# Performance work log

Measured on AMD Instinct MI355X. Metric: run time of the kernel, lower is better.

Reference implementation:

```python
import jax, jax.numpy as jnp
import numpy as np
from jax import lax

R = 2  # upscale factor


def setup_inputs() -> dict:
    key = jax.random.key(0)
    k1, k2, k3 = jax.random.split(key, 3)
    x = jax.random.normal(k1, (16, 192, 192, 64), dtype=jnp.float32)
    # Conv2D kernel: HWIO, filters = r*r*64 = 256
    W = jax.random.normal(k2, (3, 3, 64, 256), dtype=jnp.float32) * 0.05
    b = jax.random.normal(k3, (256,), dtype=jnp.float32) * 0.05
    return {"x": x, "W": W, "b": b}


def reference(x, W, b):
    # Conv2D, stride 1, 'same' padding, NHWC/HWIO
    y = lax.conv_general_dilated(
        x, W, window_strides=(1, 1), padding="SAME",
        dimension_numbers=("NHWC", "HWIO", "NHWC")) + b
    # phase_shift: O[B, i*r+q, j*r+p, k] = y[B, i, j, k*r*r + p*r + q]
    B, a, bdim, c = y.shape
    cp = c // (R * R)
    y = y.reshape(B, a, bdim, cp, R, R)          # [B,a,b,k,p,q]
    y = jnp.transpose(y, (0, 1, 5, 2, 4, 3))     # [B,a,q,b,p,k]
    return y.reshape(B, a * R, bdim * R, cp)
```

## Files before the change

### kernel.cpp

```cpp
#include <hip/hip_runtime.h>
#include <stdint.h>

typedef short bf16x8 __attribute__((ext_vector_type(8)));
typedef float f32x4  __attribute__((ext_vector_type(4)));

#define GLOAD_LDS16(gp, lp) \
    __builtin_amdgcn_global_load_lds((const __attribute__((address_space(1))) void*)(gp), \
                                     (__attribute__((address_space(3))) void*)(lp), 16, 0, 0)

__device__ __forceinline__ uint32_t bfbits(float f) {
    uint32_t u = __builtin_bit_cast(uint32_t, f);
    u += 0x7FFFu + ((u >> 16) & 1u);
    return u >> 16;
}
__device__ __forceinline__ uint32_t pk2(float a, float b) {
    return bfbits(a) | (bfbits(b) << 16);
}

__global__ void prep_kernel(const float* __restrict__ x, short* __restrict__ xb,
                            const float* __restrict__ W, short* __restrict__ Wt) {
    const int b = blockIdx.x;
    if (b < 2048) {
        const int total = 16 * 194 * 194 * 8;
        for (int i = b * 256 + threadIdx.x; i < total; i += 2048 * 256) {
            int g  = i & 7;
            int t  = i >> 3;
            int wp = t % 194; t /= 194;
            int hp = t % 194;
            int nn = t / 194;
            uint4 r = {0u, 0u, 0u, 0u};
            if (hp >= 1 && hp <= 192 && wp >= 1 && wp <= 192) {
                const float* s = x + (((size_t)nn * 192 + (hp - 1)) * 192 + (wp - 1)) * 64 + g * 8;
                f32x4 a = __builtin_nontemporal_load((const f32x4*)s);
                f32x4 bb = __builtin_nontemporal_load((const f32x4*)(s + 4));
                r.x = pk2(a[0], a[1]); r.y = pk2(a[2], a[3]);
                r.z = pk2(bb[0], bb[1]); r.w = pk2(bb[2], bb[3]);
            }
            *(uint4*)(xb + (size_t)i * 8) = r;
        }
    } else {
        int idx = (b - 2048) * 256 + threadIdx.x;
        if (idx < 147456) {
            int t  = idx >> 14;
            int r  = idx & 16383;
            int c  = r >> 12;
            int j  = (r >> 6) & 63;
            int ic = r & 63;
            Wt[idx] = (short)bfbits(W[(t * 64 + ic) * 256 + j * 4 + c]);
        }
    }
}

#define NRING 7
#define ASLOT_B 8448
#define B_OFF   (NRING * ASLOT_B)
#define SMEM_SHORTS ((B_OFF + 2 * 8192) / 2)

__global__ __launch_bounds__(256, 2) void conv_ps_kernel(
    const short* __restrict__ xb, const short* __restrict__ Wt,
    const float* __restrict__ bias, float* __restrict__ out)
{
    __shared__ short smem[SMEM_SHORTS];

    const int tid   = threadIdx.x;
    const int lane  = tid & 63;
    const int wv    = tid >> 6;
    const int row_l = lane & 15;
    const int grp   = lane >> 4;
    const int b7    = row_l & 7;

    const int raw = blockIdx.x;
    const int lb  = (raw & 7) * 192 + (raw >> 3);
    const int c    = lb & 3;
    const int wt   = (lb >> 2) % 3;
    const int hseg = (lb / 12) % 8;
    const int n    = lb / 96;
    const int w0   = wt * 64;
    const int hbase = hseg * 24;
    const int q = c & 1, p = (c >> 1) & 1;

    const short* wsrc = Wt + c * 4096;

    auto issueB = [&](int tap, int buf) {
        #pragma unroll
        for (int r = 0; r < 2; ++r) {
            int cch = tid + r * 256;
            int j = cch >> 3, s = cch & 7, ss = s ^ (j & 7);
            GLOAD_LDS16(wsrc + tap * 16384 + j * 64 + ss * 8,
                        (char*)smem + B_OFF + buf * 8192 + (wv * 64 + r * 256) * 16);
        }
    };
    auto issueA = [&](int row) {
        int rowc = row > 192 ? 192 : row;
        int slot = (row + 1) % NRING;
        size_t rbase = ((size_t)n * 194 + (rowc + 1)) * 194;
        #pragma unroll
        for (int r = 0; r < 2; ++r) {
            int cch = wv * 132 + r * 64 + lane;
            int wpos = cch >> 3, g = cch & 7, gs = g ^ (wpos & 7);
            GLOAD_LDS16(xb + (rbase + (w0 + wpos)) * 64 + gs * 8,
                        (char*)smem + slot * ASLOT_B + (wv * 132 + r * 64) * 16);
        }
        if (lane < 4) {
            int cch = wv * 132 + 128 + lane;
            int wpos = cch >> 3, g = cch & 7, gs = g ^ (wpos & 7);
            GLOAD_LDS16(xb + (rbase + (w0 + wpos)) * 64 + gs * 8,
                        (char*)smem + slot * ASLOT_B + (wv * 132 + 128) * 16);
        }
    };

    issueB(0, 0);
    #pragma unroll
    for (int r = 0; r < 5; ++r) issueA(hbase - 1 + r);
    asm volatile("s_waitcnt vmcnt(0)" ::: "memory");
    __builtin_amdgcn_sched_barrier(0);
    __syncthreads();

    f32x4 bv4[4];
    #pragma unroll
    for (int nt = 0; nt < 4; ++nt) {
        const int j0 = nt * 16 + grp * 4;
        #pragma unroll
        for (int jv = 0; jv < 4; ++jv)
            bv4[nt][jv] = bias[(j0 + jv) * 4 + c];
    }

    f32x4 accA[4][4], accB[4][4];

#define SCHB __builtin_amdgcn_sched_barrier(0)

#define COMPUTE_TAP(ACC, DY, DX, BUF) { \
    const int rd = row_l + (DX); \
    const int a7 = rd & 7; \
    const int aB = sl[DY] * 4224 + rd * 64; \
    const short* bbase = smem + B_OFF / 2 + (BUF) * 4096 + row_l * 64; \
    _Pragma("unroll") for (int ks = 0; ks < 2; ++ks) { \
        const int kg = ks * 4 + grp; \
        const short* ap = &smem[aB + ((kg ^ a7) << 3)]; \
        const short* bp = bbase + ((kg ^ b7) << 3); \
        bf16x8 af[4], bfr[4]; \
        _Pragma("unroll") for (int mt = 0; mt < 4; ++mt) af[mt]  = *(const bf16x8*)(ap + mt * 1024); \
        _Pragma("unroll") for (int nt = 0; nt < 4; ++nt) bfr[nt] = *(const bf16x8*)(bp + nt * 1024); \
        _Pragma("unroll") for (int mt = 0; mt < 4; ++mt) \
            _Pragma("unroll") for (int nt = 0; nt < 4; ++nt) \
                ACC[mt][nt] = __builtin_amdgcn_mfma_f32_16x16x32_bf16( \
                    bfr[nt], af[mt], ACC[mt][nt], 0, 0, 0); \
    } }

#define ST2(ACCO, S) { \
    const int mt_ = (S) >> 1, n0_ = ((S) & 1) * 2; \
    float* po_ = out + ((rowb_o + 2 * (w0 + mt_ * 16 + row_l) + p) * 64 + grp * 4); \
    __builtin_nontemporal_store(ACCO[mt_][n0_],     (f32x4*)(po_ + n0_ * 16)); \
    __builtin_nontemporal_store(ACCO[mt_][n0_ + 1], (f32x4*)(po_ + (n0_ + 1) * 16)); }

#define TAPX(ACC, K, DY, DX, PAR, VM, EXTRA, STS) \
    __builtin_amdgcn_s_barrier(); SCHB; \
    issueB(((K) + 1) % 9, ((PAR) + (K) + 1) & 1); \
    EXTRA; SCHB; \
    STS; SCHB; \
    asm volatile("s_waitcnt vmcnt(" #VM ")" ::: "memory"); SCHB; \
    __builtin_amdgcn_s_barrier(); SCHB; \
    COMPUTE_TAP(ACC, DY, DX, ((PAR) + (K)) & 1)

#define TILE_HEAD(ACC, ITV) \
    const int h0 = hbase + (ITV) * 4; \
    int sl[3]; \
    _Pragma("unroll") for (int dy = 0; dy < 3; ++dy) sl[dy] = (h0 + wv + dy) % NRING; \
    _Pragma("unroll") for (int i = 0; i < 4; ++i) \
        _Pragma("unroll") for (int j = 0; j < 4; ++j) ACC[i][j] = bv4[j];

#define STEADY_TILE(ACC, ACCO, ITV, PAR) { \
    TILE_HEAD(ACC, ITV); \
    const long rowb_o = ((long)(n * 384 + 2 * (h0 - 4 + wv) + q)) * 384; \
    TAPX(ACC, 0, 0, 0, PAR, 10, { issueA(h0 + 4); issueA(h0 + 5); }, ST2(ACCO, 0)); \
    TAPX(ACC, 1, 0, 1, PAR, 12, {}, ST2(ACCO, 1)); \
    TAPX(ACC, 2, 0, 2, PAR,  6, {}, ST2(ACCO, 2)); \
    TAPX(ACC, 3, 1, 0, PAR,  9, { issueA(h0 + 6); }, ST2(ACCO, 3)); \
    TAPX(ACC, 4, 1, 1, PAR,  9, {}, ST2(ACCO, 4)); \
    TAPX(ACC, 5, 1, 2, PAR,  6, {}, ST2(ACCO, 5)); \
    TAPX(ACC, 6, 2, 0, PAR,  9, { issueA(h0 + 7); }, ST2(ACCO, 6)); \
    TAPX(ACC, 7, 2, 1, PAR,  9, {}, ST2(ACCO, 7)); \
    TAPX(ACC, 8, 2, 2, PAR,  4, {}, {}); }

    {
        TILE_HEAD(accA, 0);
        TAPX(accA, 0, 0, 0, 0, 8, { issueA(h0 + 4); issueA(h0 + 5); }, {});
        TAPX(accA, 1, 0, 1, 0, 8, {}, {});
        TAPX(accA, 2, 0, 2, 0, 2, {}, {});
        TAPX(accA, 3, 1, 0, 0, 5, { issueA(h0 + 6); }, {});
        TAPX(accA, 4, 1, 1, 0, 5, {}, {});
        TAPX(accA, 5, 1, 2, 0, 2, {}, {});
        TAPX(accA, 6, 2, 0, 0, 5, { issueA(h0 + 7); }, {});
        TAPX(accA, 7, 2, 1, 0, 5, {}, {});
        TAPX(accA, 8, 2, 2, 0, 2, {}, {});
    }
    #pragma unroll 1
    for (int it2 = 1; it2 < 5; it2 += 2) {
        STEADY_TILE(accB, accA, it2, 1);
        STEADY_TILE(accA, accB, it2 + 1, 0);
    }
    STEADY_TILE(accB, accA, 5, 1);
    {
        const int h = hbase + 20 + wv;
        const long rowb = ((long)(n * 384 + 2 * h + q)) * 384;
        #pragma unroll
        for (int mt = 0; mt < 4; ++mt) {
            float* po = out + ((rowb + 2 * (w0 + mt * 16 + row_l) + p) * 64 + grp * 4);
            #pragma unroll
            for (int nt = 0; nt < 4; ++nt)
                __builtin_nontemporal_store(accB[mt][nt], (f32x4*)(po + nt * 16));
        }
    }
#undef STEADY_TILE
#undef TILE_HEAD
#undef TAPX
#undef ST2
#undef COMPUTE_TAP
#undef SCHB
}

extern "C" void kernel_launch(void* const* d_in, const int* in_sizes, int n_in,
                              void* d_out, int out_size, void* d_ws, size_t ws_size,
                              hipStream_t stream) {
    const float* x = (const float*)d_in[0];
    const float* W = (const float*)d_in[1];
    const float* b = (const float*)d_in[2];
    float* out = (float*)d_out;

    const size_t xb_bytes = (size_t)16 * 194 * 194 * 64 * 2;
    short* xbuf = (short*)d_ws;
    short* Wt   = (short*)((char*)d_ws + xb_bytes);

    hipLaunchKernelGGL(prep_kernel, dim3(2624), dim3(256), 0, stream, x, xbuf, W, Wt);
    hipLaunchKernelGGL(conv_ps_kernel, dim3(1536), dim3(256), 0, stream, xbuf, Wt, b, out);
}
```

Measured before the change: 223.4 us.

## Prefetch next tap's A fragments from LDS into double-buffered registers

Splits the per-tap LDS reads so that the A (input) fragments for the next filter tap are read into a second register set while the current tap's MFMAs run. The two sets alternate between taps, and the first tap of each tile is prefetched at the end of the previous tile. The aim is to hide LDS read latency behind MFMA execution within the barrier-separated tap schedule. In exchange, live VGPRs rise by about 64 registers. That risks lower occupancy or spills, and the early reads must not run ahead of the vmcnt waits that guard the ring buffer.

```diff
diff --git a/kernel.cpp b/kernel.cpp
--- a/kernel.cpp
+++ b/kernel.cpp
@@ -126,25 +126,18 @@
     }
 
     f32x4 accA[4][4], accB[4][4];
+    bf16x8 af0[2][4], af1[2][4];
 
 #define SCHB __builtin_amdgcn_sched_barrier(0)
 
-#define COMPUTE_TAP(ACC, DY, DX, BUF) { \
-    const int rd = row_l + (DX); \
-    const int a7 = rd & 7; \
-    const int aB = sl[DY] * 4224 + rd * 64; \
-    const short* bbase = smem + B_OFF / 2 + (BUF) * 4096 + row_l * 64; \
+#define READ_AF(DST, SLOT, DX) { \
+    const int rd_ = row_l + (DX); \
+    const int a7_ = rd_ & 7; \
+    const int aB_ = (SLOT) * 4224 + rd_ * 64; \
     _Pragma("unroll") for (int ks = 0; ks < 2; ++ks) { \
-        const int kg = ks * 4 + grp; \
-        const short* ap = &smem[aB + ((kg ^ a7) << 3)]; \
-        const short* bp = bbase + ((kg ^ b7) << 3); \
-        bf16x8 af[4], bfr[4]; \
-        _Pragma("unroll") for (int mt = 0; mt < 4; ++mt) af[mt]  = *(const bf16x8*)(ap + mt * 1024); \
-        _Pragma("unroll") for (int nt = 0; nt < 4; ++nt) bfr[nt] = *(const bf16x8*)(bp + nt * 1024); \
-        _Pragma("unroll") for (int mt = 0; mt < 4; ++mt) \
-            _Pragma("unroll") for (int nt = 0; nt < 4; ++nt) \
-                ACC[mt][nt] = __builtin_amdgcn_mfma_f32_16x16x32_bf16( \
-                    bfr[nt], af[mt], ACC[mt][nt], 0, 0, 0); \
+        const short* ap_ = &smem[aB_ + (((ks * 4 + grp) ^ a7_) << 3)]; \
+        _Pragma("unroll") for (int mt_ = 0; mt_ < 4; ++mt_) \
+            DST[ks][mt_] = *(const bf16x8*)(ap_ + mt_ * 1024); \
     } }
 
 #define ST2(ACCO, S) { \
@@ -153,53 +146,74 @@
     __builtin_nontemporal_store(ACCO[mt_][n0_],     (f32x4*)(po_ + n0_ * 16)); \
     __builtin_nontemporal_store(ACCO[mt_][n0_ + 1], (f32x4*)(po_ + (n0_ + 1) * 16)); }
 
-#define TAPX(ACC, K, DY, DX, PAR, VM, EXTRA, STS) \
+#define TAPX(ACC, K, PAR, VM, EXTRA, STS, AFC, AFN, NSLOT, NDX) \
     __builtin_amdgcn_s_barrier(); SCHB; \
     issueB(((K) + 1) % 9, ((PAR) + (K) + 1) & 1); \
     EXTRA; SCHB; \
     STS; SCHB; \
     asm volatile("s_waitcnt vmcnt(" #VM ")" ::: "memory"); SCHB; \
     __builtin_amdgcn_s_barrier(); SCHB; \
-    COMPUTE_TAP(ACC, DY, DX, ((PAR) + (K)) & 1)
+    { \
+        bf16x8 bfr[2][4]; \
+        const short* bbase_ = smem + B_OFF / 2 + ((((PAR) + (K)) & 1)) * 4096 + row_l * 64; \
+        _Pragma("unroll") for (int ks = 0; ks < 2; ++ks) { \
+            const short* bp_ = bbase_ + (((ks * 4 + grp) ^ b7) << 3); \
+            _Pragma("unroll") for (int nt_ = 0; nt_ < 4; ++nt_) \
+                bfr[ks][nt_] = *(const bf16x8*)(bp_ + nt_ * 1024); \
+        } \
+        READ_AF(AFN, NSLOT, NDX); \
+        _Pragma("unroll") for (int ks = 0; ks < 2; ++ks) \
+            _Pragma("unroll") for (int mt_ = 0; mt_ < 4; ++mt_) \
+                _Pragma("unroll") for (int nt_ = 0; nt_ < 4; ++nt_) \
+                    ACC[mt_][nt_] = __builtin_amdgcn_mfma_f32_16x16x32_bf16( \
+                        bfr[ks][nt_], AFC[ks][mt_], ACC[mt_][nt_], 0, 0, 0); \
+    }
 
 #define TILE_HEAD(ACC, ITV) \
     const int h0 = hbase + (ITV) * 4; \
     int sl[3]; \
     _Pragma("unroll") for (int dy = 0; dy < 3; ++dy) sl[dy] = (h0 + wv + dy) % NRING; \
+    const int nsl0 = (h0 + 4 + wv) % NRING; \
+    (void)nsl0; \
     _Pragma("unroll") for (int i = 0; i < 4; ++i) \
         _Pragma("unroll") for (int j = 0; j < 4; ++j) ACC[i][j] = bv4[j];
 
-#define STEADY_TILE(ACC, ACCO, ITV, PAR) { \
+#define STEADY_TILE(ACC, ACCO, ITV, PAR, AFE, AFO) { \
     TILE_HEAD(ACC, ITV); \
     const long rowb_o = ((long)(n * 384 + 2 * (h0 - 4 + wv) + q)) * 384; \
-    TAPX(ACC, 0, 0, 0, PAR, 10, { issueA(h0 + 4); issueA(h0 + 5); }, ST2(ACCO, 0)); \
-    TAPX(ACC, 1, 0, 1, PAR, 12, {}, ST2(ACCO, 1)); \
-    TAPX(ACC, 2, 0, 2, PAR,  6, {}, ST2(ACCO, 2)); \
-    TAPX(ACC, 3, 1, 0, PAR,  9, { issueA(h0 + 6); }, ST2(ACCO, 3)); \
-    TAPX(ACC, 4, 1, 1, PAR,  9, {}, ST2(ACCO, 4)); \
-    TAPX(ACC, 5, 1, 2, PAR,  6, {}, ST2(ACCO, 5)); \
-    TAPX(ACC, 6, 2, 0, PAR,  9, { issueA(h0 + 7); }, ST2(ACCO, 6)); \
-    TAPX(ACC, 7, 2, 1, PAR,  9, {}, ST2(ACCO, 7)); \
-    TAPX(ACC, 8, 2, 2, PAR,  4, {}, {}); }
+    TAPX(ACC, 0, PAR, 10, { issueA(h0 + 4); issueA(h0 + 5); }, ST2(ACCO, 0), AFE, AFO, sl[0], 1); \
+    TAPX(ACC, 1, PAR, 12, {}, ST2(ACCO, 1), AFO, AFE, sl[0], 2); \
+    TAPX(ACC, 2, PAR,  6, {}, ST2(ACCO, 2), AFE, AFO, sl[1], 0); \
+    TAPX(ACC, 3, PAR,  9, { issueA(h0 + 6); }, ST2(ACCO, 3), AFO, AFE, sl[1], 1); \
+    TAPX(ACC, 4, PAR,  9, {}, ST2(ACCO, 4), AFE, AFO, sl[1], 2); \
+    TAPX(ACC, 5, PAR,  6, {}, ST2(ACCO, 5), AFO, AFE, sl[2], 0); \
+    TAPX(ACC, 6, PAR,  9, { issueA(h0 + 7); }, ST2(ACCO, 6), AFE, AFO, sl[2], 1); \
+    TAPX(ACC, 7, PAR,  9, {}, ST2(ACCO, 7), AFO, AFE, sl[2], 2); \
+    TAPX(ACC, 8, PAR,  4, {}, {}, AFE, AFO, nsl0, 0); }
+
+    {
+        const int psl = (hbase + wv) % NRING;
+        READ_AF(af0, psl, 0);
+    }
 
     {
         TILE_HEAD(accA, 0);
-        TAPX(accA, 0, 0, 0, 0, 8, { issueA(h0 + 4); issueA(h0 + 5); }, {});
-        TAPX(accA, 1, 0, 1, 0, 8, {}, {});
-        TAPX(accA, 2, 0, 2, 0, 2, {}, {});
-        TAPX(accA, 3, 1, 0, 0, 5, { issueA(h0 + 6); }, {});
-        TAPX(accA, 4, 1, 1, 0, 5, {}, {});
-        TAPX(accA, 5, 1, 2, 0, 2, {}, {});
-        TAPX(accA, 6, 2, 0, 0, 5, { issueA(h0 + 7); }, {});
-        TAPX(accA, 7, 2, 1, 0, 5, {}, {});
-        TAPX(accA, 8, 2, 2, 0, 2, {}, {});
+        TAPX(accA, 0, 0, 8, { issueA(h0 + 4); issueA(h0 + 5); }, {}, af0, af1, sl[0], 1);
+        TAPX(accA, 1, 0, 8, {}, {}, af1, af0, sl[0], 2);
+        TAPX(accA, 2, 0, 2, {}, {}, af0, af1, sl[1], 0);
+        TAPX(accA, 3, 0, 5, { issueA(h0 + 6); }, {}, af1, af0, sl[1], 1);
+        TAPX(accA, 4, 0, 5, {}, {}, af0, af1, sl[1], 2);
+        TAPX(accA, 5, 0, 2, {}, {}, af1, af0, sl[2], 0);
+        TAPX(accA, 6, 0, 5, { issueA(h0 + 7); }, {}, af0, af1, sl[2], 1);
+        TAPX(accA, 7, 0, 5, {}, {}, af1, af0, sl[2], 2);
+        TAPX(accA, 8, 0, 2, {}, {}, af0, af1, nsl0, 0);
     }
     #pragma unroll 1
     for (int it2 = 1; it2 < 5; it2 += 2) {
-        STEADY_TILE(accB, accA, it2, 1);
-        STEADY_TILE(accA, accB, it2 + 1, 0);
-    }
-    STEADY_TILE(accB, accA, 5, 1);
+        STEADY_TILE(accB, accA, it2, 1, af1, af0);
+        STEADY_TILE(accA, accB, it2 + 1, 0, af0, af1);
+    }
+    STEADY_TILE(accB, accA, 5, 1, af1, af0);
     {
         const int h = hbase + 20 + wv;
         const long rowb = ((long)(n * 384 + 2 * h + q)) * 384;
@@ -215,7 +229,7 @@
 #undef TILE_HEAD
 #undef TAPX
 #undef ST2
-#undef COMPUTE_TAP
+#undef READ_AF
 #undef SCHB
 }
 
```

Result: slower. 234.1 us (+4.8%).

## Fuse fp32-to-bf16 input conversion and padding into conv kernel via register staging

Applied to the files above, without the earlier changes.

Removes the separate prep pass that wrote a padded bf16 copy of the input. The conv kernel now loads fp32 rows into registers, converts and zero-pads them in-kernel, and writes them swizzled into the LDS ring, interleaved with MFMA taps under retuned waitcnt values. This saves a full read plus write of the activation tensor. In exchange it reads fp32 (twice the bytes per tile, with halo rows re-read by neighbouring blocks), uses 9 extra vector registers for staging, and adds VALU conversion work inside the main loop.

```diff
diff --git a/kernel.cpp b/kernel.cpp
--- a/kernel.cpp
+++ b/kernel.cpp
@@ -17,37 +17,15 @@
     return bfbits(a) | (bfbits(b) << 16);
 }
 
-__global__ void prep_kernel(const float* __restrict__ x, short* __restrict__ xb,
-                            const float* __restrict__ W, short* __restrict__ Wt) {
-    const int b = blockIdx.x;
-    if (b < 2048) {
-        const int total = 16 * 194 * 194 * 8;
-        for (int i = b * 256 + threadIdx.x; i < total; i += 2048 * 256) {
-            int g  = i & 7;
-            int t  = i >> 3;
-            int wp = t % 194; t /= 194;
-            int hp = t % 194;
-            int nn = t / 194;
-            uint4 r = {0u, 0u, 0u, 0u};
-            if (hp >= 1 && hp <= 192 && wp >= 1 && wp <= 192) {
-                const float* s = x + (((size_t)nn * 192 + (hp - 1)) * 192 + (wp - 1)) * 64 + g * 8;
-                f32x4 a = __builtin_nontemporal_load((const f32x4*)s);
-                f32x4 bb = __builtin_nontemporal_load((const f32x4*)(s + 4));
-                r.x = pk2(a[0], a[1]); r.y = pk2(a[2], a[3]);
-                r.z = pk2(bb[0], bb[1]); r.w = pk2(bb[2], bb[3]);
-            }
-            *(uint4*)(xb + (size_t)i * 8) = r;
-        }
-    } else {
-        int idx = (b - 2048) * 256 + threadIdx.x;
-        if (idx < 147456) {
-            int t  = idx >> 14;
-            int r  = idx & 16383;
-            int c  = r >> 12;
-            int j  = (r >> 6) & 63;
-            int ic = r & 63;
-            Wt[idx] = (short)bfbits(W[(t * 64 + ic) * 256 + j * 4 + c]);
-        }
+__global__ void wt_kernel(const float* __restrict__ W, short* __restrict__ Wt) {
+    int idx = blockIdx.x * 256 + threadIdx.x;
+    if (idx < 147456) {
+        int t  = idx >> 14;
+        int r  = idx & 16383;
+        int c  = r >> 12;
+        int j  = (r >> 6) & 63;
+        int ic = r & 63;
+        Wt[idx] = (short)bfbits(W[(t * 64 + ic) * 256 + j * 4 + c]);
     }
 }
 
@@ -57,7 +35,7 @@
 #define SMEM_SHORTS ((B_OFF + 2 * 8192) / 2)
 
 __global__ __launch_bounds__(256, 2) void conv_ps_kernel(
-    const short* __restrict__ xb, const short* __restrict__ Wt,
+    const float* __restrict__ x, const short* __restrict__ Wt,
     const float* __restrict__ bias, float* __restrict__ out)
 {
     __shared__ short smem[SMEM_SHORTS];
@@ -90,28 +68,55 @@
                         (char*)smem + B_OFF + buf * 8192 + (wv * 64 + r * 256) * 16);
         }
     };
-    auto issueA = [&](int row) {
-        int rowc = row > 192 ? 192 : row;
-        int slot = (row + 1) % NRING;
-        size_t rbase = ((size_t)n * 194 + (rowc + 1)) * 194;
-        #pragma unroll
-        for (int r = 0; r < 2; ++r) {
-            int cch = wv * 132 + r * 64 + lane;
-            int wpos = cch >> 3, g = cch & 7, gs = g ^ (wpos & 7);
-            GLOAD_LDS16(xb + (rbase + (w0 + wpos)) * 64 + gs * 8,
-                        (char*)smem + slot * ASLOT_B + (wv * 132 + r * 64) * 16);
+
+    f32x4 stg[9];
+
+#define STGLOAD(BASE, J0, NJ) { \
+    _Pragma("unroll") for (int j_ = (J0); j_ < (J0) + (NJ); ++j_) { \
+        int cid_ = tid + j_ * 256; int cc_ = cid_ < 2112 ? cid_ : 0; \
+        int rl_ = cc_ / 1056, rem_ = cc_ - rl_ * 1056; \
+        int wpos_ = rem_ >> 4, c4_ = rem_ & 15; \
+        int hy_ = (BASE) + rl_; \
+        int hyc_ = hy_ > 191 ? 191 : hy_; \
+        int wg_ = w0 - 1 + wpos_; \
+        int wgc_ = wg_ < 0 ? 0 : (wg_ > 191 ? 191 : wg_); \
+        stg[j_] = *(const f32x4*)(x + (((size_t)n * 192 + hyc_) * 192 + wgc_) * 64 + c4_ * 4); \
+    } }
+
+#define CVTW(BASE) { \
+    _Pragma("unroll") for (int j_ = 0; j_ < 9; ++j_) { \
+        int cid_ = tid + j_ * 256; \
+        if (cid_ < 2112) { \
+            int rl_ = cid_ / 1056, rem_ = cid_ - rl_ * 1056; \
+            int wpos_ = rem_ >> 4, c4_ = rem_ & 15; \
+            int hy_ = (BASE) + rl_; \
+            int wg_ = w0 - 1 + wpos_; \
+            uint2 pr_; pr_.x = pk2(stg[j_][0], stg[j_][1]); pr_.y = pk2(stg[j_][2], stg[j_][3]); \
+            if ((unsigned)wg_ >= 192u || hy_ > 191) { pr_.x = 0; pr_.y = 0; } \
+            int slot_ = (hy_ + 1) % NRING; \
+            *(uint2*)&smem[slot_ * 4224 + wpos_ * 64 + \
+                           (((c4_ >> 1) ^ (wpos_ & 7)) << 3) + (c4_ & 1) * 4] = pr_; \
+        } } }
+
+    issueB(0, 0);
+    #pragma unroll 3
+    for (int k = 0; k < 21; ++k) {
+        int cid = tid + k * 256;
+        if (cid < 5280) {
+            int rl = cid / 1056, rem = cid - rl * 1056;
+            int wpos = rem >> 4, c4 = rem & 15;
+            int hy = hbase - 1 + rl;
+            int wg = w0 - 1 + wpos;
+            int hyc = hy < 0 ? 0 : hy;
+            int wgc = wg < 0 ? 0 : (wg > 191 ? 191 : wg);
+            f32x4 v = *(const f32x4*)(x + (((size_t)n * 192 + hyc) * 192 + wgc) * 64 + c4 * 4);
+            uint2 pr; pr.x = pk2(v[0], v[1]); pr.y = pk2(v[2], v[3]);
+            if (hy < 0 || (unsigned)wg >= 192u) { pr.x = 0; pr.y = 0; }
+            int slot = (hy + 1 + NRING) % NRING;
+            *(uint2*)&smem[slot * 4224 + wpos * 64 +
+                           (((c4 >> 1) ^ (wpos & 7)) << 3) + (c4 & 1) * 4] = pr;
         }
-        if (lane < 4) {
-            int cch = wv * 132 + 128 + lane;
-            int wpos = cch >> 3, g = cch & 7, gs = g ^ (wpos & 7);
-            GLOAD_LDS16(xb + (rbase + (w0 + wpos)) * 64 + gs * 8,
-                        (char*)smem + slot * ASLOT_B + (wv * 132 + 128) * 16);
-        }
-    };
-
-    issueB(0, 0);
-    #pragma unroll
-    for (int r = 0; r < 5; ++r) issueA(hbase - 1 + r);
+    }
     asm volatile("s_waitcnt vmcnt(0)" ::: "memory");
     __builtin_amdgcn_sched_barrier(0);
     __syncthreads();
@@ -153,12 +158,12 @@
     __builtin_nontemporal_store(ACCO[mt_][n0_],     (f32x4*)(po_ + n0_ * 16)); \
     __builtin_nontemporal_store(ACCO[mt_][n0_ + 1], (f32x4*)(po_ + (n0_ + 1) * 16)); }
 
-#define TAPX(ACC, K, DY, DX, PAR, VM, EXTRA, STS) \
+#define TAPX(ACC, K, DY, DX, PAR, VMSTR, EXTRA, STS) \
     __builtin_amdgcn_s_barrier(); SCHB; \
     issueB(((K) + 1) % 9, ((PAR) + (K) + 1) & 1); \
     EXTRA; SCHB; \
     STS; SCHB; \
-    asm volatile("s_waitcnt vmcnt(" #VM ")" ::: "memory"); SCHB; \
+    asm volatile("s_waitcnt " VMSTR ::: "memory"); SCHB; \
     __builtin_amdgcn_s_barrier(); SCHB; \
     COMPUTE_TAP(ACC, DY, DX, ((PAR) + (K)) & 1)
 
@@ -172,27 +177,27 @@
 #define STEADY_TILE(ACC, ACCO, ITV, PAR) { \
     TILE_HEAD(ACC, ITV); \
     const long rowb_o = ((long)(n * 384 + 2 * (h0 - 4 + wv) + q)) * 384; \
-    TAPX(ACC, 0, 0, 0, PAR, 10, { issueA(h0 + 4); issueA(h0 + 5); }, ST2(ACCO, 0)); \
-    TAPX(ACC, 1, 0, 1, PAR, 12, {}, ST2(ACCO, 1)); \
-    TAPX(ACC, 2, 0, 2, PAR,  6, {}, ST2(ACCO, 2)); \
-    TAPX(ACC, 3, 1, 0, PAR,  9, { issueA(h0 + 6); }, ST2(ACCO, 3)); \
-    TAPX(ACC, 4, 1, 1, PAR,  9, {}, ST2(ACCO, 4)); \
-    TAPX(ACC, 5, 1, 2, PAR,  6, {}, ST2(ACCO, 5)); \
-    TAPX(ACC, 6, 2, 0, PAR,  9, { issueA(h0 + 7); }, ST2(ACCO, 6)); \
-    TAPX(ACC, 7, 2, 1, PAR,  9, {}, ST2(ACCO, 7)); \
-    TAPX(ACC, 8, 2, 2, PAR,  4, {}, {}); }
+    TAPX(ACC, 0, 0, 0, PAR, "vmcnt(9)",              STGLOAD(h0 + 4, 0, 5), ST2(ACCO, 0)); \
+    TAPX(ACC, 1, 0, 1, PAR, "vmcnt(15)",             STGLOAD(h0 + 4, 5, 4), ST2(ACCO, 1)); \
+    TAPX(ACC, 2, 0, 2, PAR, "vmcnt(10)",             {}, ST2(ACCO, 2)); \
+    TAPX(ACC, 3, 1, 0, PAR, "vmcnt(6) lgkmcnt(0)",   CVTW(h0 + 4), ST2(ACCO, 3)); \
+    TAPX(ACC, 4, 1, 1, PAR, "vmcnt(11)",             STGLOAD(h0 + 6, 0, 5), ST2(ACCO, 4)); \
+    TAPX(ACC, 5, 1, 2, PAR, "vmcnt(15)",             STGLOAD(h0 + 6, 5, 4), ST2(ACCO, 5)); \
+    TAPX(ACC, 6, 2, 0, PAR, "vmcnt(10)",             {}, ST2(ACCO, 6)); \
+    TAPX(ACC, 7, 2, 1, PAR, "vmcnt(6) lgkmcnt(0)",   CVTW(h0 + 6), ST2(ACCO, 7)); \
+    TAPX(ACC, 8, 2, 2, PAR, "vmcnt(4)",              {}, {}); }
 
     {
         TILE_HEAD(accA, 0);
-        TAPX(accA, 0, 0, 0, 0, 8, { issueA(h0 + 4); issueA(h0 + 5); }, {});
-        TAPX(accA, 1, 0, 1, 0, 8, {}, {});
-        TAPX(accA, 2, 0, 2, 0, 2, {}, {});
-        TAPX(accA, 3, 1, 0, 0, 5, { issueA(h0 + 6); }, {});
-        TAPX(accA, 4, 1, 1, 0, 5, {}, {});
-        TAPX(accA, 5, 1, 2, 0, 2, {}, {});
-        TAPX(accA, 6, 2, 0, 0, 5, { issueA(h0 + 7); }, {});
-        TAPX(accA, 7, 2, 1, 0, 5, {}, {});
-        TAPX(accA, 8, 2, 2, 0, 2, {}, {});
+        TAPX(accA, 0, 0, 0, 0, "vmcnt(7)",            STGLOAD(h0 + 4, 0, 5), {});
+        TAPX(accA, 1, 0, 1, 0, "vmcnt(11)",           STGLOAD(h0 + 4, 5, 4), {});
+        TAPX(accA, 2, 0, 2, 0, "vmcnt(6)",            {}, {});
+        TAPX(accA, 3, 1, 0, 0, "vmcnt(2) lgkmcnt(0)", CVTW(h0 + 4), {});
+        TAPX(accA, 4, 1, 1, 0, "vmcnt(7)",            STGLOAD(h0 + 6, 0, 5), {});
+        TAPX(accA, 5, 1, 2, 0, "vmcnt(11)",           STGLOAD(h0 + 6, 5, 4), {});
+        TAPX(accA, 6, 2, 0, 0, "vmcnt(6)",            {}, {});
+        TAPX(accA, 7, 2, 1, 0, "vmcnt(2) lgkmcnt(0)", CVTW(h0 + 6), {});
+        TAPX(accA, 8, 2, 2, 0, "vmcnt(2)",            {}, {});
     }
     #pragma unroll 1
     for (int it2 = 1; it2 < 5; it2 += 2) {
@@ -216,6 +221,8 @@
 #undef TAPX
 #undef ST2
 #undef COMPUTE_TAP
+#undef CVTW
+#undef STGLOAD
 #undef SCHB
 }
 
@@ -226,11 +233,8 @@
     const float* W = (const float*)d_in[1];
     const float* b = (const float*)d_in[2];
     float* out = (float*)d_out;
-
-    const size_t xb_bytes = (size_t)16 * 194 * 194 * 64 * 2;
-    short* xbuf = (short*)d_ws;
-    short* Wt   = (short*)((char*)d_ws + xb_bytes);
-
-    hipLaunchKernelGGL(prep_kernel, dim3(2624), dim3(256), 0, stream, x, xbuf, W, Wt);
-    hipLaunchKernelGGL(conv_ps_kernel, dim3(1536), dim3(256), 0, stream, xbuf, Wt, b, out);
-}
+    short* Wt = (short*)d_ws;
+
+    hipLaunchKernelGGL(wt_kernel, dim3(576), dim3(256), 0, stream, W, Wt);
+    hipLaunchKernelGGL(conv_ps_kernel, dim3(1536), dim3(256), 0, stream, x, Wt, b, out);
+}
```

Measured after the change: 513.7 us. 2.3x slower.
